# Optimization experiments

Measured on AMD Instinct MI355X. Metric: run time of the kernel, lower is better.

## Reference

```python
import jax, jax.numpy as jnp
import numpy as np

# Module constants (from __init__)
RADIUS = 1.0
VOXEL_SIZE = (0.16, 0.16)
PC_RANGE = (0.0, -25.6)
K = 4  # sample_points

M, N, C = 16384, 4096, 64
GRID = 320  # (51.2 - 0) / 0.16


def setup_inputs() -> dict:
    key = jax.random.key(0)
    k1, k2, k3, k4, k5 = jax.random.split(key, 5)
    pillar_feature = jax.random.normal(k1, (M, C), dtype=jnp.float32)
    # coors: (batch_id, z, y, x); single batch, z=0, y/x in BEV grid
    ys = jax.random.randint(k2, (M,), 0, GRID, dtype=jnp.int32)
    xs = jax.random.randint(k3, (M,), 0, GRID, dtype=jnp.int32)
    zeros = jnp.zeros((M,), dtype=jnp.int32)
    coors = jnp.stack([zeros, zeros, ys, xs], axis=1)  # [M, 4]
    seg_feats = jax.random.normal(k4, (N, C), dtype=jnp.float32)
    # seg points uniform in the BEV extent, z arbitrary (zeroed in forward)
    u = jax.random.uniform(k5, (N, 3), dtype=jnp.float32)
    seg_points = jnp.stack([
        u[:, 0] * 51.2 + 0.0,
        u[:, 1] * 51.2 - 25.6,
        u[:, 2] * 5.0 - 3.0,
    ], axis=1)  # [N, 3]
    return {"pillar_feature": pillar_feature, "coors": coors,
            "seg_feats": seg_feats, "seg_points": seg_points}


def _ball_query_idx(query_xy, pts_xy, radius, k_samples):
    """Replicates pointnet2/mmcv ball_query: for each query, the first
    k_samples in-radius point indices (scan order), slots padded with the
    first found index; all-zeros when no neighbor exists."""
    # [M, N] squared xy distance
    d2 = jnp.sum((query_xy[:, None, :] - pts_xy[None, :, :]) ** 2, axis=-1)
    within = d2 < radius * radius                       # [M, N]
    order = jnp.cumsum(within.astype(jnp.int32), axis=1)  # 1-based rank among in-radius pts
    slots = []
    for k in range(k_samples):  # small fixed K
        match = within & (order == k + 1)               # [M, N]
        has = jnp.any(match, axis=1)                    # [M]
        j = jnp.argmax(match, axis=1).astype(jnp.int32) # 0 when no match (CUDA zero-init)
        slots.append((has, j))
    first = slots[0][1]                                 # [M]
    idx = jnp.stack([jnp.where(h, j, first) for h, j in slots], axis=1)  # [M, K]
    return idx


def reference(pillar_feature, coors, seg_feats, seg_points):
    # get_pillar_center: x = (coors[:,3]+0.5)*vx + pc_x, y = (coors[:,2]+0.5)*vy + pc_y
    cf = coors.astype(jnp.float32)
    px = (cf[:, 3] + 0.5) * VOXEL_SIZE[0] + PC_RANGE[0]
    py = (cf[:, 2] + 0.5) * VOXEL_SIZE[1] + PC_RANGE[1]
    pillar_xy = jnp.stack([px, py], axis=1)             # [M, 2] (z zeroed in original)
    pts_xy = seg_points[:, :2]                          # z zeroed in original

    idx = _ball_query_idx(pillar_xy, pts_xy, RADIUS, K)  # [M, K] int32
    flag = (jnp.sum(idx, axis=1) > 0).astype(pillar_feature.dtype)  # [M]

    grouped = seg_feats[idx]                            # [M, K, C] gather
    pooled = jnp.max(grouped, axis=1)                   # max-pool over K samples
    return pillar_feature + pooled * flag[:, None]
```

## Files before the change

kernel.cpp:

```cpp
#include <hip/hip_runtime.h>

#define NPTS  4096
#define MQ    16384
#define CF    64
#define GRIDC 32
#define NCELLS (GRIDC * GRIDC)
#define CAP   20
#define INVCELL 0.625f
#define SENT  0x7fffffff
#define TPB   1024
#define NBLK  512
#define QPB   (MQ / NBLK)
#define WPB   (TPB / 64)
#define QPW   (QPB / WPB)

__global__ __launch_bounds__(TPB) void k_all(
    const float* __restrict__ pillar,
    const int*   __restrict__ coors,
    const float* __restrict__ segf,
    const float* __restrict__ segp,
    float* __restrict__ out)
{
    __shared__ float2 sxy[NPTS];
    __shared__ int scnt[NCELLS];
    __shared__ unsigned short sbkt[NCELLS * CAP];

    const int tid = threadIdx.x;

    scnt[tid & (NCELLS - 1)] = 0;
    __syncthreads();

    for (int p = tid; p < NPTS; p += TPB) {
        const float px = segp[3 * p + 0];
        const float py = segp[3 * p + 1];
        sxy[p] = make_float2(px, py);
        int ix = (int)(px * INVCELL);
        int iy = (int)((py + 25.6f) * INVCELL);
        ix = min(max(ix, 0), GRIDC - 1);
        iy = min(max(iy, 0), GRIDC - 1);
        const int slot = atomicAdd(&scnt[iy * GRIDC + ix], 1);
        if (slot < CAP) sbkt[(iy * GRIDC + ix) * CAP + slot] = (unsigned short)p;
    }
    __syncthreads();

    const int wave = tid >> 6;
    const int lane = tid & 63;
    const int lc = lane / 20;
    const int sl = lane - lc * 20;

    for (int it = 0; it < QPW; ++it) {
        const int q = blockIdx.x * QPB + wave * QPW + it;
        const int cx = coors[4 * q + 3];
        const int cy = coors[4 * q + 2];
        const float qx = __fadd_rn(__fmul_rn(__fadd_rn((float)cx, 0.5f), 0.16f), 0.0f);
        const float qy = __fadd_rn(__fmul_rn(__fadd_rn((float)cy, 0.5f), 0.16f), -25.6f);
        const int icx = (int)(qx * INVCELL);
        const int icy = (int)((qy + 25.6f) * INVCELL);

        int c0 = SENT, c1 = SENT, c2 = SENT;
#pragma unroll
        for (int b = 0; b < 3; ++b) {
            int cand = SENT;
            if (lc < 3) {
                const int j = 3 * b + lc;
                const int iy2 = icy + j / 3 - 1;
                const int ix2 = icx + j % 3 - 1;
                if (ix2 >= 0 && ix2 < GRIDC && iy2 >= 0 && iy2 < GRIDC) {
                    const int cell = iy2 * GRIDC + ix2;
                    int cnt = scnt[cell];
                    cnt = cnt > CAP ? CAP : cnt;
                    if (sl < cnt) {
                        const int id = sbkt[cell * CAP + sl];
                        const float2 e = sxy[id];
                        const float dx = __fsub_rn(qx, e.x);
                        const float dy = __fsub_rn(qy, e.y);
                        const float d2 = __fadd_rn(__fmul_rn(dx, dx), __fmul_rn(dy, dy));
                        if (d2 < 1.0f) cand = id;
                    }
                }
            }
            if (cand < c2) {
                if (cand < c1) {
                    c2 = c1;
                    if (cand < c0) { c1 = c0; c0 = cand; } else { c1 = cand; }
                } else { c2 = cand; }
            }
        }

        int v0 = c0, v1 = c1, v2 = c2, v3 = SENT;
#pragma unroll
        for (int off = 1; off < 64; off <<= 1) {
            const int w0 = __shfl_xor(v0, off);
            const int w1 = __shfl_xor(v1, off);
            const int w2 = __shfl_xor(v2, off);
            const int w3 = __shfl_xor(v3, off);
            const int t0 = min(v0, w3);
            const int t1 = min(v1, w2);
            const int t2 = min(v2, w1);
            const int t3 = min(v3, w0);
            const int a0 = min(t0, t2), a2 = max(t0, t2);
            const int a1 = min(t1, t3), a3 = max(t1, t3);
            v0 = min(a0, a1); v1 = max(a0, a1);
            v2 = min(a2, a3); v3 = max(a2, a3);
        }

        int i0, i1, i2, i3, flag;
        if (v0 == SENT) {
            i0 = i1 = i2 = i3 = 0; flag = 0;
        } else {
            i0 = v0;
            i1 = (v1 == SENT) ? v0 : v1;
            i2 = (v2 == SENT) ? v0 : v2;
            i3 = (v3 == SENT) ? v0 : v3;
            flag = (i0 + i1 + i2 + i3) > 0;
        }

        float m = 0.0f;
        if (flag) {
            const float a = segf[i0 * CF + lane];
            const float b2 = segf[i1 * CF + lane];
            const float c = segf[i2 * CF + lane];
            const float d = segf[i3 * CF + lane];
            m = fmaxf(fmaxf(a, b2), fmaxf(c, d));
        }
        out[q * CF + lane] = pillar[q * CF + lane] + m;
    }
}

extern "C" void kernel_launch(void* const* d_in, const int* in_sizes, int n_in,
                              void* d_out, int out_size, void* d_ws, size_t ws_size,
                              hipStream_t stream) {
    const float* pillar = (const float*)d_in[0];
    const int*   coors  = (const int*)d_in[1];
    const float* segf   = (const float*)d_in[2];
    const float* segp   = (const float*)d_in[3];
    float* out = (float*)d_out;

    k_all<<<NBLK, TPB, 0, stream>>>(pillar, coors, segf, segp, out);
}
```

Measured before the change: 70.44 us.

## Process two queries per wave with half-wave scans and packed 16-bit shuffles

Each wave now handles two queries at once, one per 32-lane half. Each half scans all 180 candidate slots of the 3x3 cell neighbourhood in 6 rounds and keeps the 4 smallest in-radius indices per lane, instead of 3. The cross-lane top-4 merge uses 5 shuffle stages over 32 lanes with indices packed as 16-bit pairs, so it needs two shuffles per stage instead of four. The feature gather and output write use float2 per lane. The per-wave query loop is removed, since QPB=32 equals 16 waves times 2 queries; this keeps the same total work with fewer sequential shuffle reductions but adds register pressure.

Result: faster. 68.38 us (-2.9%).

```diff
diff --git a/kernel.cpp b/kernel.cpp
--- a/kernel.cpp
+++ b/kernel.cpp
@@ -7,12 +7,11 @@
 #define NCELLS (GRIDC * GRIDC)
 #define CAP   20
 #define INVCELL 0.625f
-#define SENT  0x7fffffff
+#define SENT16 0xFFFF
 #define TPB   1024
 #define NBLK  512
 #define QPB   (MQ / NBLK)
 #define WPB   (TPB / 64)
-#define QPW   (QPB / WPB)
 
 __global__ __launch_bounds__(TPB) void k_all(
     const float* __restrict__ pillar,
@@ -45,86 +44,92 @@
 
     const int wave = tid >> 6;
     const int lane = tid & 63;
-    const int lc = lane / 20;
-    const int sl = lane - lc * 20;
+    const int h  = lane >> 5;
+    const int hl = lane & 31;
 
-    for (int it = 0; it < QPW; ++it) {
-        const int q = blockIdx.x * QPB + wave * QPW + it;
-        const int cx = coors[4 * q + 3];
-        const int cy = coors[4 * q + 2];
-        const float qx = __fadd_rn(__fmul_rn(__fadd_rn((float)cx, 0.5f), 0.16f), 0.0f);
-        const float qy = __fadd_rn(__fmul_rn(__fadd_rn((float)cy, 0.5f), 0.16f), -25.6f);
-        const int icx = (int)(qx * INVCELL);
-        const int icy = (int)((qy + 25.6f) * INVCELL);
+    const int q = blockIdx.x * QPB + wave * 2 + h;
+    const int2 cc = *(const int2*)(&coors[4 * q + 2]);
+    const float qx = __fadd_rn(__fmul_rn(__fadd_rn((float)cc.y, 0.5f), 0.16f), 0.0f);
+    const float qy = __fadd_rn(__fmul_rn(__fadd_rn((float)cc.x, 0.5f), 0.16f), -25.6f);
+    const int icx = (int)(qx * INVCELL);
+    const int icy = (int)((qy + 25.6f) * INVCELL);
 
-        int c0 = SENT, c1 = SENT, c2 = SENT;
+    int c0 = SENT16, c1 = SENT16, c2 = SENT16, c3 = SENT16;
 #pragma unroll
-        for (int b = 0; b < 3; ++b) {
-            int cand = SENT;
-            if (lc < 3) {
-                const int j = 3 * b + lc;
-                const int iy2 = icy + j / 3 - 1;
-                const int ix2 = icx + j % 3 - 1;
-                if (ix2 >= 0 && ix2 < GRIDC && iy2 >= 0 && iy2 < GRIDC) {
-                    const int cell = iy2 * GRIDC + ix2;
-                    int cnt = scnt[cell];
-                    cnt = cnt > CAP ? CAP : cnt;
-                    if (sl < cnt) {
-                        const int id = sbkt[cell * CAP + sl];
-                        const float2 e = sxy[id];
-                        const float dx = __fsub_rn(qx, e.x);
-                        const float dy = __fsub_rn(qy, e.y);
-                        const float d2 = __fadd_rn(__fmul_rn(dx, dx), __fmul_rn(dy, dy));
-                        if (d2 < 1.0f) cand = id;
-                    }
+    for (int b = 0; b < 6; ++b) {
+        const int s = b * 32 + hl;
+        int cand = SENT16;
+        if (s < 180) {
+            const int j  = s / 20;
+            const int sl = s - j * 20;
+            const int iy2 = icy + j / 3 - 1;
+            const int ix2 = icx + j % 3 - 1;
+            if (ix2 >= 0 && ix2 < GRIDC && iy2 >= 0 && iy2 < GRIDC) {
+                const int cell = iy2 * GRIDC + ix2;
+                int cnt = scnt[cell];
+                cnt = cnt > CAP ? CAP : cnt;
+                if (sl < cnt) {
+                    const int id = sbkt[cell * CAP + sl];
+                    const float2 e = sxy[id];
+                    const float dx = __fsub_rn(qx, e.x);
+                    const float dy = __fsub_rn(qy, e.y);
+                    const float d2 = __fadd_rn(__fmul_rn(dx, dx), __fmul_rn(dy, dy));
+                    if (d2 < 1.0f) cand = id;
                 }
             }
+        }
+        if (cand < c3) {
             if (cand < c2) {
+                c3 = c2;
                 if (cand < c1) {
                     c2 = c1;
                     if (cand < c0) { c1 = c0; c0 = cand; } else { c1 = cand; }
                 } else { c2 = cand; }
-            }
+            } else { c3 = cand; }
         }
+    }
 
-        int v0 = c0, v1 = c1, v2 = c2, v3 = SENT;
+    unsigned int A = (unsigned int)c0 | ((unsigned int)c1 << 16);
+    unsigned int B = (unsigned int)c2 | ((unsigned int)c3 << 16);
 #pragma unroll
-        for (int off = 1; off < 64; off <<= 1) {
-            const int w0 = __shfl_xor(v0, off);
-            const int w1 = __shfl_xor(v1, off);
-            const int w2 = __shfl_xor(v2, off);
-            const int w3 = __shfl_xor(v3, off);
-            const int t0 = min(v0, w3);
-            const int t1 = min(v1, w2);
-            const int t2 = min(v2, w1);
-            const int t3 = min(v3, w0);
-            const int a0 = min(t0, t2), a2 = max(t0, t2);
-            const int a1 = min(t1, t3), a3 = max(t1, t3);
-            v0 = min(a0, a1); v1 = max(a0, a1);
-            v2 = min(a2, a3); v3 = max(a2, a3);
-        }
+    for (int off = 1; off < 32; off <<= 1) {
+        const unsigned int Ax = (unsigned int)__shfl_xor((int)A, off);
+        const unsigned int Bx = (unsigned int)__shfl_xor((int)B, off);
+        const int w0 = (int)(Ax & 0xFFFFu), w1 = (int)(Ax >> 16);
+        const int w2 = (int)(Bx & 0xFFFFu), w3 = (int)(Bx >> 16);
+        const int t0 = min(c0, w3), t1 = min(c1, w2);
+        const int t2 = min(c2, w1), t3 = min(c3, w0);
+        const int a0 = min(t0, t2), a2 = max(t0, t2);
+        const int a1 = min(t1, t3), a3 = max(t1, t3);
+        c0 = min(a0, a1); c1 = max(a0, a1);
+        c2 = min(a2, a3); c3 = max(a2, a3);
+        A = (unsigned int)c0 | ((unsigned int)c1 << 16);
+        B = (unsigned int)c2 | ((unsigned int)c3 << 16);
+    }
 
-        int i0, i1, i2, i3, flag;
-        if (v0 == SENT) {
-            i0 = i1 = i2 = i3 = 0; flag = 0;
-        } else {
-            i0 = v0;
-            i1 = (v1 == SENT) ? v0 : v1;
-            i2 = (v2 == SENT) ? v0 : v2;
-            i3 = (v3 == SENT) ? v0 : v3;
-            flag = (i0 + i1 + i2 + i3) > 0;
-        }
+    int i0, i1, i2, i3, flag;
+    if (c0 == SENT16) {
+        i0 = i1 = i2 = i3 = 0; flag = 0;
+    } else {
+        i0 = c0;
+        i1 = (c1 == SENT16) ? c0 : c1;
+        i2 = (c2 == SENT16) ? c0 : c2;
+        i3 = (c3 == SENT16) ? c0 : c3;
+        flag = (i0 + i1 + i2 + i3) > 0;
+    }
 
-        float m = 0.0f;
-        if (flag) {
-            const float a = segf[i0 * CF + lane];
-            const float b2 = segf[i1 * CF + lane];
-            const float c = segf[i2 * CF + lane];
-            const float d = segf[i3 * CF + lane];
-            m = fmaxf(fmaxf(a, b2), fmaxf(c, d));
-        }
-        out[q * CF + lane] = pillar[q * CF + lane] + m;
+    const int col = 2 * hl;
+    float2 m2 = make_float2(0.0f, 0.0f);
+    if (flag) {
+        const float2 a = *(const float2*)(&segf[i0 * CF + col]);
+        const float2 b = *(const float2*)(&segf[i1 * CF + col]);
+        const float2 c = *(const float2*)(&segf[i2 * CF + col]);
+        const float2 d = *(const float2*)(&segf[i3 * CF + col]);
+        m2.x = fmaxf(fmaxf(a.x, b.x), fmaxf(c.x, d.x));
+        m2.y = fmaxf(fmaxf(a.y, b.y), fmaxf(c.y, d.y));
     }
+    const float2 p2 = *(const float2*)(&pillar[q * CF + col]);
+    *(float2*)(&out[q * CF + col]) = make_float2(p2.x + m2.x, p2.y + m2.y);
 }
 
 extern "C" void kernel_launch(void* const* d_in, const int* in_sizes, int n_in,
```
